# Kernel optimization log

Measured on AMD Instinct MI355X. Metric: run time of the kernel, lower is better.

## Reference

```python
import jax, jax.numpy as jnp
import numpy as np

MAX_STEPS = 20  # cap on ACT pondering steps; torch loop is data-dependent
EPS = 0.01


def setup_inputs() -> dict:
    key = jax.random.key(0)
    ks = jax.random.split(key, 10)
    I, H, O = 1024, 2048, 1024
    s = 1.0 / np.sqrt(H).astype(np.float32)
    return {
        "x": jax.random.normal(ks[0], (I,), jnp.float32),
        "h": jax.random.normal(ks[1], (H,), jnp.float32) * 0.1,
        "c": jax.random.normal(ks[2], (H,), jnp.float32) * 0.1,
        "W_ih": jax.random.normal(ks[3], (4 * H, I + 1), jnp.float32) * s,
        "W_hh": jax.random.normal(ks[4], (4 * H, H), jnp.float32) * s,
        "b_ih": jax.random.normal(ks[5], (4 * H,), jnp.float32) * s,
        "b_hh": jax.random.normal(ks[6], (4 * H,), jnp.float32) * s,
        "w_halt": jax.random.normal(ks[7], (H,), jnp.float32) * s,
        "b_halt": jnp.ones((1,), jnp.float32),  # module sets fc_halt.bias = [1.0]
        "W_out": jax.random.normal(ks[8], (O, H), jnp.float32) * s,
        "b_out": jax.random.normal(ks[9], (O,), jnp.float32) * s,
    }


def _forward(x, h, c, W_ih, W_hh, b_ih, b_hh, w_halt, b_halt, W_out, b_out):
    # First step sees input [1, x]; all subsequent steps see [0, x].
    flags = jnp.zeros((MAX_STEPS,), x.dtype).at[0].set(1.0)

    def step(carry, flag):
        h_t, c_t, cum = carry
        inp = jnp.concatenate([flag[None], x])  # [1+I]
        gates = W_ih @ inp + b_ih + W_hh @ h_t + b_hh  # [4H], torch gate order i,f,g,o
        i, f, g, o = jnp.split(gates, 4)
        c_new = jax.nn.sigmoid(f) * c_t + jax.nn.sigmoid(i) * jnp.tanh(g)
        h_new = jax.nn.sigmoid(o) * jnp.tanh(c_new)
        p = jax.nn.sigmoid(jnp.dot(w_halt, h_new) + b_halt[0])
        cum_new = cum + p
        out_t = W_out @ h_new + b_out
        return (h_new, c_new, cum_new), (h_new, c_new, out_t, cum_new)

    _, (states, cells, outs, cums) = jax.lax.scan(
        step, (h, c, jnp.float32(0.0)), flags)

    thresh = 1.0 - EPS
    halted = cums >= thresh                       # cum halting prob is monotone
    prev_halted = jnp.concatenate([jnp.zeros((1,), bool), halted[:-1]])
    valid = jnp.cumsum(prev_halted.astype(jnp.int32)) == 0  # steps torch actually ran
    b_hard = halted & valid                       # exactly the first halting step
    b_hard = b_hard.at[-1].set(b_hard[-1] | ~jnp.any(halted))  # force halt at cap
    # Straight-through Binarize: forward = hard 0/1, grad flows to cum halting probs
    soft = jnp.where(valid, cums, 0.0)
    b = soft + jax.lax.stop_gradient(b_hard.astype(cums.dtype) - soft)

    output = jnp.einsum('to,t->o', outs, b)   # mv(outputs_tensor, binarized)
    h_out = jnp.einsum('th,t->h', states, b)
    c_out = jnp.einsum('th,t->h', cells, b)
    ponder = jnp.sum(jnp.where(valid, 1.0 - b, 0.0))  # = n, # of non-halt steps
    return output, h_out, c_out, ponder


def reference(x, h, c, W_ih, W_hh, b_ih, b_hh, w_halt, b_halt, W_out, b_out):
    return _forward(x, h, c, W_ih, W_hh, b_ih, b_hh, w_halt, b_halt, W_out, b_out)
```

## Files before the change

kernel.cpp:

```cpp
#include <hip/hip_runtime.h>


#define NB    1024
#define BT    256
#define CPB   2
#define HDIM  2048
#define IDIM  1024
#define G4    8192
#define MAXS  20

static_assert(NB * CPB == HDIM, "columns must tile H");

__device__ __attribute__((aligned(16))) float g_h[2][HDIM];
__device__ float g_c[HDIM];
__device__ float g_part[2][NB];
__device__ float g_z[G4];
__device__ float g_cums[MAXS];
__device__ int   g_done, g_tstar, g_curbuf;

__device__ __forceinline__ float wave_reduce(float v) {
  #pragma unroll
  for (int off = 32; off; off >>= 1) v += __shfl_xor(v, off, 64);
  return v;
}
__device__ __forceinline__ float sigf(float v) {
  return 1.0f / (1.0f + expf(-v));
}
__device__ __forceinline__ float dot4(float4 a, float4 b) {
  return a.x * b.x + a.y * b.y + a.z * b.z + a.w * b.w;
}

__device__ __forceinline__ void step_body(
    int cur, bool first, const float4* __restrict__ hsrc,
    const float* __restrict__ c_in, const float* __restrict__ W_ih,
    const float* __restrict__ W_hh, const float* __restrict__ w_halt,
    float za, float zb)
{
  const int tid  = threadIdx.x;
  const int w    = tid >> 6;
  const int lane = tid & 63;
  const int j0   = blockIdx.x * CPB;
  const int ra   = w * HDIM + j0;
  const int rb   = ra + 1;

  __shared__ float4 hs[HDIM / 4];
  __shared__ float  gsm[4][CPB];
  __shared__ float  pvs[CPB];

  hs[tid]       = hsrc[tid];
  hs[tid + 256] = hsrc[tid + 256];
  __syncthreads();

  const float4* Whh4 = reinterpret_cast<const float4*>(W_hh);
  const float4* WA4  = Whh4 + (size_t)ra * (HDIM / 4);
  const float4* WB4  = Whh4 + (size_t)rb * (HDIM / 4);
  float4 wa[8], wb[8];
  #pragma unroll
  for (int t = 0; t < 8; ++t) {
    const int idx = t * 64 + lane;
    wa[t] = WA4[idx];
    wb[t] = WB4[idx];
  }
  float sa = 0.f, sb = 0.f;
  #pragma unroll
  for (int t = 0; t < 8; ++t) {
    const float4 hv = hs[t * 64 + lane];
    sa += dot4(wa[t], hv);
    sb += dot4(wb[t], hv);
  }
  sa = wave_reduce(sa);
  sb = wave_reduce(sb);
  if (lane == 0) {
    gsm[w][0] = za + sa;
    gsm[w][1] = zb + sb;
  }
  __syncthreads();

  if (tid < CPB) {
    const int j = j0 + tid;
    const float gi = gsm[0][tid], gf = gsm[1][tid];
    const float gg = gsm[2][tid], go = gsm[3][tid];
    const float co = first ? c_in[j] : g_c[j];
    const float cn = sigf(gf) * co + sigf(gi) * tanhf(gg);
    const float hn = sigf(go) * tanhf(cn);
    g_c[j]      = cn;
    g_h[cur][j] = hn;
    pvs[tid]    = w_halt[j] * hn;
  }
  __syncthreads();
  if (tid == 0) g_part[cur][blockIdx.x] = pvs[0] + pvs[1];
}

__global__ __launch_bounds__(BT, 4) void fb_step0(
    const float* __restrict__ x,    const float* __restrict__ h_in,
    const float* __restrict__ c_in, const float* __restrict__ W_ih,
    const float* __restrict__ W_hh, const float* __restrict__ b_ih,
    const float* __restrict__ b_hh, const float* __restrict__ w_halt)
{
  const int tid  = threadIdx.x;
  const int w    = tid >> 6;
  const int lane = tid & 63;
  const int j0   = blockIdx.x * CPB;
  const int ra   = w * HDIM + j0;
  const int rb   = ra + 1;

  if (blockIdx.x == 0 && tid == 0) g_done = 0;

  const float* Wa = W_ih + (size_t)ra * (IDIM + 1);
  const float* Wb = W_ih + (size_t)rb * (IDIM + 1);
  float za = 0.f, zb = 0.f;
  #pragma unroll
  for (int k = 0; k < 2; ++k) {
    float xv[8], va[8], vb[8];
    #pragma unroll
    for (int t = 0; t < 8; ++t) {
      const int c = (k * 8 + t) * 64 + lane;
      xv[t] = x[c];
      va[t] = Wa[1 + c];
      vb[t] = Wb[1 + c];
    }
    #pragma unroll
    for (int t = 0; t < 8; ++t) { za += va[t] * xv[t]; zb += vb[t] * xv[t]; }
  }
  za = wave_reduce(za) + b_ih[ra] + b_hh[ra];
  zb = wave_reduce(zb) + b_ih[rb] + b_hh[rb];
  if (lane == 0) {
    g_z[ra] = za;
    g_z[rb] = zb;
  }
  step_body(0, true,
            reinterpret_cast<const float4*>(h_in), c_in, W_ih, W_hh, w_halt,
            za + Wa[0], zb + Wb[0]);
}

__global__ __launch_bounds__(BT, 4) void fb_stepN(int step,
    const float* __restrict__ c_in, const float* __restrict__ W_ih,
    const float* __restrict__ W_hh, const float* __restrict__ w_halt,
    const float* __restrict__ b_halt)
{
  if (g_done) return;

  const int tid  = threadIdx.x;
  const int w    = tid >> 6;
  const int lane = tid & 63;
  const int prev = (step - 1) & 1;

  __shared__ float red[4];
  {
    float ps = g_part[prev][tid]       + g_part[prev][tid + 256]
             + g_part[prev][tid + 512] + g_part[prev][tid + 768];
    ps = wave_reduce(ps);
    if (lane == 0) red[w] = ps;
    __syncthreads();
    const float ssum = (red[0] + red[1]) + (red[2] + red[3]);
    const float p    = sigf(ssum + b_halt[0]);
    const float cum  = (step >= 2 ? g_cums[step - 2] : 0.f) + p;
    if (blockIdx.x == 0 && tid == 0) g_cums[step - 1] = cum;
    if (cum >= 0.99f) {
      if (blockIdx.x == 0 && tid == 0) {
        g_done = 1; g_tstar = step - 1; g_curbuf = prev;
      }
      return;
    }
  }
  __syncthreads();

  const int ra = w * HDIM + blockIdx.x * CPB;
  const float za = (lane == 0) ? g_z[ra]     : 0.f;
  const float zb = (lane == 0) ? g_z[ra + 1] : 0.f;
  step_body(step & 1, false,
            reinterpret_cast<const float4*>((const float*)g_h[prev]),
            c_in, W_ih, W_hh, w_halt, za, zb);
}

__global__ __launch_bounds__(BT, 4) void fb_final(
    const float* __restrict__ W_out, const float* __restrict__ b_out,
    float* __restrict__ out)
{
  const int tid = threadIdx.x, w = tid >> 6, lane = tid & 63;
  const int j0  = blockIdx.x * CPB;
  const int curbuf = g_done ? g_curbuf : (MAXS - 1) & 1;
  const int tstar  = g_done ? g_tstar  : (MAXS - 1);
  const float* hf  = g_h[curbuf];

  __shared__ float red[4];
  const int r = blockIdx.x;
  const float4* Wo4 = reinterpret_cast<const float4*>(W_out)
                      + (size_t)r * (HDIM / 4);
  const float4* hf4 = reinterpret_cast<const float4*>(hf);
  const float4 wv0 = Wo4[tid], wv1 = Wo4[tid + 256];
  const float4 hv0 = hf4[tid], hv1 = hf4[tid + 256];
  float acc = dot4(wv0, hv0) + dot4(wv1, hv1);
  acc = wave_reduce(acc);
  if (lane == 0) red[w] = acc;
  __syncthreads();
  if (tid == 0) out[r] = (red[0] + red[1]) + (red[2] + red[3]) + b_out[r];

  if (tid < CPB) {
    const int j = j0 + tid;
    out[1024 + j] = hf[j];
    out[3072 + j] = g_c[j];
  }
  if (blockIdx.x == 0 && tid == CPB) out[5120] = (float)tstar;
}

extern "C" void kernel_launch(void* const* d_in, const int* in_sizes, int n_in,
                              void* d_out, int out_size, void* d_ws, size_t ws_size,
                              hipStream_t stream) {
  (void)in_sizes; (void)n_in; (void)d_ws; (void)ws_size; (void)out_size;
  const float* x      = (const float*)d_in[0];
  const float* h      = (const float*)d_in[1];
  const float* c      = (const float*)d_in[2];
  const float* W_ih   = (const float*)d_in[3];
  const float* W_hh   = (const float*)d_in[4];
  const float* b_ih   = (const float*)d_in[5];
  const float* b_hh   = (const float*)d_in[6];
  const float* w_halt = (const float*)d_in[7];
  const float* b_halt = (const float*)d_in[8];
  const float* W_out  = (const float*)d_in[9];
  const float* b_out  = (const float*)d_in[10];
  float* out = (float*)d_out;

  fb_step0<<<dim3(NB), dim3(BT), 0, stream>>>(x, h, c, W_ih, W_hh,
                                              b_ih, b_hh, w_halt);
  for (int s = 1; s < MAXS; ++s)
    fb_stepN<<<dim3(NB), dim3(BT), 0, stream>>>(s, c, W_ih, W_hh,
                                                w_halt, b_halt);
  fb_final<<<dim3(NB), dim3(BT), 0, stream>>>(W_out, b_out, out);
}
```

Baseline: 189.9 us.

## Collapse pondering steps 2+ into one single-block tail kernel

Replaces the 18 per-step grid launches for steps 2..19 with a dedicated step-1 kernel plus one single-block kernel. The tail kernel exits immediately if halting has already happened; otherwise it runs the remaining LSTM steps serially inside one workgroup. This removes the launch overhead of many early-exit kernels when ACT halts early. The cost is a very slow fallback if the halting threshold is not reached early, because one block then streams all of W_hh on every step.

```diff
diff --git a/kernel.cpp b/kernel.cpp
--- a/kernel.cpp
+++ b/kernel.cpp
@@ -15,7 +15,7 @@
 __device__ float g_c[HDIM];
 __device__ float g_part[2][NB];
 __device__ float g_z[G4];
-__device__ float g_cums[MAXS];
+__device__ float g_cum0;
 __device__ int   g_done, g_tstar, g_curbuf;
 
 __device__ __forceinline__ float wave_reduce(float v) {
@@ -32,9 +32,8 @@
 
 __device__ __forceinline__ void step_body(
     int cur, bool first, const float4* __restrict__ hsrc,
-    const float* __restrict__ c_in, const float* __restrict__ W_ih,
-    const float* __restrict__ W_hh, const float* __restrict__ w_halt,
-    float za, float zb)
+    const float* __restrict__ c_in, const float* __restrict__ W_hh,
+    const float* __restrict__ w_halt, float za, float zb)
 {
   const int tid  = threadIdx.x;
   const int w    = tid >> 6;
@@ -129,48 +128,97 @@
     g_z[rb] = zb;
   }
   step_body(0, true,
-            reinterpret_cast<const float4*>(h_in), c_in, W_ih, W_hh, w_halt,
+            reinterpret_cast<const float4*>(h_in), c_in, W_hh, w_halt,
             za + Wa[0], zb + Wb[0]);
 }
 
-__global__ __launch_bounds__(BT, 4) void fb_stepN(int step,
-    const float* __restrict__ c_in, const float* __restrict__ W_ih,
-    const float* __restrict__ W_hh, const float* __restrict__ w_halt,
-    const float* __restrict__ b_halt)
-{
-  if (g_done) return;
-
-  const int tid  = threadIdx.x;
-  const int w    = tid >> 6;
-  const int lane = tid & 63;
-  const int prev = (step - 1) & 1;
+__global__ __launch_bounds__(BT, 4) void fb_step1(
+    const float* __restrict__ c_in, const float* __restrict__ W_hh,
+    const float* __restrict__ w_halt, const float* __restrict__ b_halt)
+{
+  const int tid  = threadIdx.x;
+  const int w    = tid >> 6;
+  const int lane = tid & 63;
 
   __shared__ float red[4];
-  {
-    float ps = g_part[prev][tid]       + g_part[prev][tid + 256]
-             + g_part[prev][tid + 512] + g_part[prev][tid + 768];
-    ps = wave_reduce(ps);
-    if (lane == 0) red[w] = ps;
-    __syncthreads();
-    const float ssum = (red[0] + red[1]) + (red[2] + red[3]);
-    const float p    = sigf(ssum + b_halt[0]);
-    const float cum  = (step >= 2 ? g_cums[step - 2] : 0.f) + p;
-    if (blockIdx.x == 0 && tid == 0) g_cums[step - 1] = cum;
-    if (cum >= 0.99f) {
-      if (blockIdx.x == 0 && tid == 0) {
-        g_done = 1; g_tstar = step - 1; g_curbuf = prev;
-      }
-      return;
-    }
+  float ps = g_part[0][tid]       + g_part[0][tid + 256]
+           + g_part[0][tid + 512] + g_part[0][tid + 768];
+  ps = wave_reduce(ps);
+  if (lane == 0) red[w] = ps;
+  __syncthreads();
+  const float p0 = sigf((red[0] + red[1]) + (red[2] + red[3]) + b_halt[0]);
+  if (blockIdx.x == 0 && tid == 0) g_cum0 = p0;
+  if (p0 >= 0.99f) {
+    if (blockIdx.x == 0 && tid == 0) { g_done = 1; g_tstar = 0; g_curbuf = 0; }
+    return;
   }
   __syncthreads();
 
   const int ra = w * HDIM + blockIdx.x * CPB;
   const float za = (lane == 0) ? g_z[ra]     : 0.f;
   const float zb = (lane == 0) ? g_z[ra + 1] : 0.f;
-  step_body(step & 1, false,
-            reinterpret_cast<const float4*>((const float*)g_h[prev]),
-            c_in, W_ih, W_hh, w_halt, za, zb);
+  step_body(1, false,
+            reinterpret_cast<const float4*>((const float*)g_h[0]),
+            c_in, W_hh, w_halt, za, zb);
+}
+
+__global__ __launch_bounds__(BT) void fb_tail(
+    const float* __restrict__ W_hh, const float* __restrict__ w_halt,
+    const float* __restrict__ b_halt)
+{
+  if (g_done) return;
+  const int tid  = threadIdx.x;
+  const int w    = tid >> 6;
+  const int lane = tid & 63;
+  const float bh = b_halt[0];
+
+  __shared__ float red[4];
+  float ps = g_part[1][tid]       + g_part[1][tid + 256]
+           + g_part[1][tid + 512] + g_part[1][tid + 768];
+  ps = wave_reduce(ps);
+  if (lane == 0) red[w] = ps;
+  __syncthreads();
+  float cum = g_cum0 + sigf((red[0] + red[1]) + (red[2] + red[3]) + bh);
+  if (cum >= 0.99f) {
+    if (tid == 0) { g_done = 1; g_tstar = 1; g_curbuf = 1; }
+    return;
+  }
+
+  __shared__ float hs2[HDIM];
+  int tstar = -1;
+  for (int s = 2; s < MAXS; ++s) {
+    const float* hp = g_h[(s - 1) & 1];
+    __syncthreads();
+    for (int i = tid; i < HDIM; i += BT) hs2[i] = hp[i];
+    __syncthreads();
+    float psum = 0.f;
+    for (int k = 0; k < HDIM / BT; ++k) {
+      const int j = tid + k * BT;
+      float gs[4];
+      #pragma unroll
+      for (int gq = 0; gq < 4; ++gq) {
+        const float* Wr = W_hh + (size_t)(gq * HDIM + j) * HDIM;
+        float acc = 0.f;
+        for (int t = 0; t < HDIM; ++t) acc += Wr[t] * hs2[t];
+        gs[gq] = g_z[gq * HDIM + j] + acc;
+      }
+      const float cn = sigf(gs[1]) * g_c[j] + sigf(gs[0]) * tanhf(gs[2]);
+      const float hn = sigf(gs[3]) * tanhf(cn);
+      g_c[j] = cn;
+      g_h[s & 1][j] = hn;
+      psum += w_halt[j] * hn;
+    }
+    __syncthreads();
+    psum = wave_reduce(psum);
+    if (lane == 0) red[w] = psum;
+    __syncthreads();
+    cum += sigf((red[0] + red[1]) + (red[2] + red[3]) + bh);
+    if (cum >= 0.99f) { tstar = s; break; }
+  }
+  if (tid == 0) {
+    const int t = (tstar >= 0) ? tstar : (MAXS - 1);
+    g_done = 1; g_tstar = t; g_curbuf = t & 1;
+  }
 }
 
 __global__ __launch_bounds__(BT, 4) void fb_final(
@@ -179,8 +227,8 @@
 {
   const int tid = threadIdx.x, w = tid >> 6, lane = tid & 63;
   const int j0  = blockIdx.x * CPB;
-  const int curbuf = g_done ? g_curbuf : (MAXS - 1) & 1;
-  const int tstar  = g_done ? g_tstar  : (MAXS - 1);
+  const int curbuf = g_curbuf;
+  const int tstar  = g_tstar;
   const float* hf  = g_h[curbuf];
 
   __shared__ float red[4];
@@ -223,8 +271,7 @@
 
   fb_step0<<<dim3(NB), dim3(BT), 0, stream>>>(x, h, c, W_ih, W_hh,
                                               b_ih, b_hh, w_halt);
-  for (int s = 1; s < MAXS; ++s)
-    fb_stepN<<<dim3(NB), dim3(BT), 0, stream>>>(s, c, W_ih, W_hh,
-                                                w_halt, b_halt);
+  fb_step1<<<dim3(NB), dim3(BT), 0, stream>>>(c, W_hh, w_halt, b_halt);
+  fb_tail <<<dim3(1),  dim3(BT), 0, stream>>>(W_hh, w_halt, b_halt);
   fb_final<<<dim3(NB), dim3(BT), 0, stream>>>(W_out, b_out, out);
 }
```

Result: faster. 167.7 us (-11.7%).
